# Optimization experiments

Measured on AMD Instinct MI355X. Metric: run time of the kernel, lower is better.

Reference implementation:

```python
import jax, jax.numpy as jnp
import numpy as np

N_NODES = 50000
N_EDGES = 800000
IN_DIM = 128
HID = 128
N_LAYERS = 3
N_CLASSES = 6
NUM_GRAPHS = 64
BN_EPS = 1e-5


def setup_inputs() -> dict:
    key = jax.random.key(0)
    ks = jax.random.split(key, 12)
    x = jax.random.normal(ks[0], (N_NODES, IN_DIM), dtype=jnp.float32)
    edge_index = jax.random.randint(ks[1], (2, N_EDGES), 0, N_NODES, dtype=jnp.int32)
    batch = jnp.sort(jax.random.randint(ks[2], (N_NODES,), 0, NUM_GRAPHS, dtype=jnp.int32))
    s = 1.0 / np.sqrt(HID)
    # stacked per-layer params (all layers are [HID, HID] since IN_DIM == HID)
    Wl = jax.random.uniform(ks[3], (N_LAYERS, HID, HID), jnp.float32, -s, s)  # lin_l (neighbor agg), has bias
    bl = jax.random.uniform(ks[4], (N_LAYERS, HID), jnp.float32, -s, s)
    Wr = jax.random.uniform(ks[5], (N_LAYERS, HID, HID), jnp.float32, -s, s)  # lin_r (root), no bias
    gamma = jnp.ones((N_LAYERS, HID), jnp.float32)
    beta = jnp.zeros((N_LAYERS, HID), jnp.float32)
    W1 = jax.random.uniform(ks[6], (HID // 2, HID), jnp.float32, -s, s)
    b1 = jax.random.uniform(ks[7], (HID // 2,), jnp.float32, -s, s)
    s2 = 1.0 / np.sqrt(HID // 2)
    W2 = jax.random.uniform(ks[8], (N_CLASSES, HID // 2), jnp.float32, -s2, s2)
    b2 = jax.random.uniform(ks[9], (N_CLASSES,), jnp.float32, -s2, s2)
    return {"x": x, "edge_index": edge_index, "batch": batch, "Wl": Wl, "bl": bl,
            "Wr": Wr, "gamma": gamma, "beta": beta, "W1": W1, "b1": b1, "W2": W2, "b2": b2}


def reference(x, edge_index, batch, Wl, bl, Wr, gamma, beta, W1, b1, W2, b2):
    src, dst = edge_index[0], edge_index[1]
    n = x.shape[0]
    # in-degree (for mean aggregation), computed once; clamp to avoid div-by-zero
    deg = jax.ops.segment_sum(jnp.ones((src.shape[0],), x.dtype), dst, num_segments=n)
    deg = jnp.maximum(deg, 1.0)[:, None]
    for l in range(N_LAYERS):
        # SAGEConv: mean-aggregate neighbor features, then lin_l(agg) + lin_r(x)
        agg = jax.ops.segment_sum(x[src], dst, num_segments=n) / deg  # [N, HID]
        h = agg @ Wl[l].T + bl[l] + x @ Wr[l].T
        # BatchNorm1d (training-mode batch statistics over nodes)
        mu = h.mean(axis=0)
        var = h.var(axis=0)
        h = (h - mu) * jax.lax.rsqrt(var + BN_EPS) * gamma[l] + beta[l]
        x = jax.nn.relu(h)  # dropout omitted (eval semantics / deterministic baseline)
    # global_mean_pool over graph ids
    pooled = jax.ops.segment_sum(x, batch, num_segments=NUM_GRAPHS)
    cnt = jax.ops.segment_sum(jnp.ones((n,), x.dtype), batch, num_segments=NUM_GRAPHS)
    pooled = pooled / jnp.maximum(cnt, 1.0)[:, None]
    # MLP head
    h = jax.nn.relu(pooled @ W1.T + b1)
    return h @ W2.T + b2
```

## Files before the change

### kernel.cpp

```cpp
#include <hip/hip_runtime.h>

#define N_NODES 50000
#define N_EDGES 800000
#define DIM 128
#define NLAYERS 3
#define NCLASSES 6
#define NGRAPHS 64
#define BN_EPS 1e-5f

#define SCAN_BLK 256
#define SCAN_NB ((N_NODES + SCAN_BLK - 1) / SCAN_BLK)

#define POOL_CHUNKS 8
#define NPART 16

#define FILL_GRPS 8
#define FILL_BPG 128
#define NODES_PER_GRP ((N_NODES + FILL_GRPS - 1) / FILL_GRPS)

typedef unsigned short ushort_t;
typedef unsigned int uint_t;
using bf16x8 = __attribute__((ext_vector_type(8))) short;
using f32x4 = __attribute__((ext_vector_type(4))) float;

__device__ __forceinline__ float bf2f(ushort_t b) {
  return __uint_as_float(((uint_t)b) << 16);
}
__device__ __forceinline__ ushort_t f2bf(float f) {
  uint_t u = __float_as_uint(f);
  u += 0x7fffu + ((u >> 16) & 1u);
  return (ushort_t)(u >> 16);
}


__global__ void k_count(const int* __restrict__ dst, int* __restrict__ cnt) {
  int e = blockIdx.x * blockDim.x + threadIdx.x;
  if (e < N_EDGES) atomicAdd(&cnt[dst[e]], 1);
}

__global__ void k_scan_a(const int* __restrict__ cnt, int* __restrict__ incl,
                         int* __restrict__ bsum) {
  __shared__ int s[SCAN_BLK];
  int i = blockIdx.x * SCAN_BLK + threadIdx.x;
  int v = (i < N_NODES) ? cnt[i] : 0;
  s[threadIdx.x] = v;
  __syncthreads();
  for (int off = 1; off < SCAN_BLK; off <<= 1) {
    int t = (threadIdx.x >= off) ? s[threadIdx.x - off] : 0;
    __syncthreads();
    s[threadIdx.x] += t;
    __syncthreads();
  }
  if (i < N_NODES) incl[i] = s[threadIdx.x];
  if (threadIdx.x == SCAN_BLK - 1) bsum[blockIdx.x] = s[SCAN_BLK - 1];
}

__global__ void k_scan_b(const int* __restrict__ bsum, int* __restrict__ boff) {
  __shared__ int s[SCAN_BLK];
  int t = threadIdx.x;
  int v = (t < SCAN_NB) ? bsum[t] : 0;
  s[t] = v;
  __syncthreads();
  for (int off = 1; off < SCAN_BLK; off <<= 1) {
    int u = (t >= off) ? s[t - off] : 0;
    __syncthreads();
    s[t] += u;
    __syncthreads();
  }
  boff[t] = s[t] - v;
}

__global__ void k_scan_c(const int* __restrict__ cnt, const int* __restrict__ incl,
                         const int* __restrict__ boff, int* __restrict__ row_ptr,
                         int* __restrict__ cursor, float* __restrict__ degf) {
  int i = blockIdx.x * SCAN_BLK + threadIdx.x;
  if (i < N_NODES) {
    int ex = incl[i] - cnt[i] + boff[blockIdx.x];
    row_ptr[i] = ex;
    cursor[i] = ex;
    degf[i] = (float)max(cnt[i], 1);
  }
  if (i == 0) row_ptr[N_NODES] = N_EDGES;
}

__global__ void k_fill2(const int* __restrict__ src, const int* __restrict__ dst,
                        int* __restrict__ cursor, int* __restrict__ col) {
  int grp = blockIdx.x & (FILL_GRPS - 1);
  int blk = blockIdx.x >> 3;
  int lo = grp * NODES_PER_GRP;
  int hi = min(lo + NODES_PER_GRP, N_NODES);
  int per = (N_EDGES + FILL_BPG - 1) / FILL_BPG;
  int es = blk * per, ee = min(es + per, N_EDGES);
  for (int e = es + (int)threadIdx.x; e < ee; e += (int)blockDim.x) {
    int d = dst[e];
    if (d >= lo && d < hi) {
      int pos = atomicAdd(&cursor[d], 1);
      col[pos] = src[e];
    }
  }
}

__global__ void k_wt2(const float* __restrict__ Wl, const float* __restrict__ Wr,
                      ushort_t* __restrict__ W2) {
  int i = blockIdx.x * blockDim.x + threadIdx.x;
  if (i >= NLAYERS * 8 * 4 * 128) return;
  int c = i & 127;
  int q = (i >> 7) & 3;
  int ks = (i >> 9) & 7;
  int l = i >> 12;
  int kbase = ks * 32 + q * 8;
  size_t obase = (size_t)l * 65536 + ks * 8192 + q * 1024 + c * 8;
#pragma unroll
  for (int kk = 0; kk < 8; ++kk) {
    int k = kbase + kk;
    float w = (k < DIM) ? Wl[(size_t)l * DIM * DIM + c * DIM + k]
                        : Wr[(size_t)l * DIM * DIM + c * DIM + (k - DIM)];
    ushort_t hi = f2bf(w);
    float lo = w - bf2f(hi);
    W2[obase + kk] = hi;
    W2[obase + 4096 + kk] = f2bf(lo);
  }
}

__global__ void k_tobf16(const float* __restrict__ x, ushort_t* __restrict__ xb) {
  int i4 = blockIdx.x * blockDim.x + threadIdx.x;
  if (i4 >= N_NODES * DIM / 4) return;
  float4 v = ((const float4*)x)[i4];
  ushort4 o;
  o.x = f2bf(v.x);
  o.y = f2bf(v.y);
  o.z = f2bf(v.z);
  o.w = f2bf(v.w);
  ((ushort4*)xb)[i4] = o;
}


__global__ void k_gather4(const ushort_t* __restrict__ xb, const int* __restrict__ row_ptr,
                          const int* __restrict__ col, const float* __restrict__ degf,
                          ushort_t* __restrict__ aggb) {
  int wid = threadIdx.x >> 6, lane = threadIdx.x & 63;
  int n = blockIdx.x * 4 + wid;
  if (n >= N_NODES) return;
  int beg = row_ptr[n], end = row_ptr[n + 1];
  int sub = lane >> 4;
  int c16 = lane & 15;
  const uint4* x4 = (const uint4*)xb;
  float a[8] = {0.f, 0.f, 0.f, 0.f, 0.f, 0.f, 0.f, 0.f};
  int p = beg + sub;
  for (; p + 12 < end; p += 16) {
    int c[4];
#pragma unroll
    for (int u = 0; u < 4; ++u) c[u] = col[p + 4 * u];
    uint4 v[4];
#pragma unroll
    for (int u = 0; u < 4; ++u) v[u] = x4[(size_t)c[u] * 16 + c16];
#pragma unroll
    for (int u = 0; u < 4; ++u) {
      a[0] += bf2f((ushort_t)(v[u].x & 0xffffu));
      a[1] += bf2f((ushort_t)(v[u].x >> 16));
      a[2] += bf2f((ushort_t)(v[u].y & 0xffffu));
      a[3] += bf2f((ushort_t)(v[u].y >> 16));
      a[4] += bf2f((ushort_t)(v[u].z & 0xffffu));
      a[5] += bf2f((ushort_t)(v[u].z >> 16));
      a[6] += bf2f((ushort_t)(v[u].w & 0xffffu));
      a[7] += bf2f((ushort_t)(v[u].w >> 16));
    }
  }
  for (; p < end; p += 4) {
    uint4 v = x4[(size_t)col[p] * 16 + c16];
    a[0] += bf2f((ushort_t)(v.x & 0xffffu));
    a[1] += bf2f((ushort_t)(v.x >> 16));
    a[2] += bf2f((ushort_t)(v.y & 0xffffu));
    a[3] += bf2f((ushort_t)(v.y >> 16));
    a[4] += bf2f((ushort_t)(v.z & 0xffffu));
    a[5] += bf2f((ushort_t)(v.z >> 16));
    a[6] += bf2f((ushort_t)(v.w & 0xffffu));
    a[7] += bf2f((ushort_t)(v.w >> 16));
  }
#pragma unroll
  for (int u = 0; u < 8; ++u) {
    a[u] += __shfl_xor(a[u], 16);
    a[u] += __shfl_xor(a[u], 32);
  }
  if (sub == 0) {
    float inv = 1.0f / degf[n];
    uint4 o;
    o.x = (uint_t)f2bf(a[0] * inv) | ((uint_t)f2bf(a[1] * inv) << 16);
    o.y = (uint_t)f2bf(a[2] * inv) | ((uint_t)f2bf(a[3] * inv) << 16);
    o.z = (uint_t)f2bf(a[4] * inv) | ((uint_t)f2bf(a[5] * inv) << 16);
    o.w = (uint_t)f2bf(a[6] * inv) | ((uint_t)f2bf(a[7] * inv) << 16);
    ((uint4*)aggb)[(size_t)n * 16 + c16] = o;
  }
}

__global__ __launch_bounds__(256) void k_mfma3(
    const ushort_t* __restrict__ aggb, const ushort_t* __restrict__ xb,
    const ushort_t* __restrict__ W2l, const float* __restrict__ bl,
    ushort_t* __restrict__ hb, float* __restrict__ sums_part) {
  __shared__ ushort_t Bs[16384];
  __shared__ float Es[4][16][65];
  __shared__ float lsums[4][256];

  int tid = threadIdx.x;
  int wave = tid >> 6, lane = tid & 63;
  int rw = blockIdx.x * 64 + wave * 16;
  int lr = lane & 15;
  int q = lane >> 4;
  int rowA = rw + lr;
  if (rowA > N_NODES - 1) rowA = N_NODES - 1;

  f32x4 acc[8];
#pragma unroll
  for (int c = 0; c < 8; ++c) acc[c] = (f32x4){0.f, 0.f, 0.f, 0.f};

#pragma unroll 1
  for (int kp = 0; kp < 4; ++kp) {
    const uint4* wsrc = (const uint4*)(W2l + (size_t)kp * 16384);
#pragma unroll
    for (int it = 0; it < 8; ++it)
      ((uint4*)Bs)[it * 256 + tid] = wsrc[it * 256 + tid];
    __syncthreads();
#pragma unroll
    for (int kh = 0; kh < 2; ++kh) {
      int ks = kp * 2 + kh;
      const ushort_t* Asrc = (ks < 4) ? aggb : xb;
      int koff = (ks & 3) * 32 + q * 8;
      bf16x8 af = *(const bf16x8*)(Asrc + (size_t)rowA * DIM + koff);
      const ushort_t* bbase = Bs + kh * 8192 + q * 1024;
#pragma unroll
      for (int cf = 0; cf < 8; ++cf) {
        int ci = cf * 16 + lr;
        bf16x8 bh = *(const bf16x8*)(bbase + ci * 8);
        bf16x8 bo = *(const bf16x8*)(bbase + 4096 + ci * 8);
        acc[cf] = __builtin_amdgcn_mfma_f32_16x16x32_bf16(af, bh, acc[cf], 0, 0, 0);
        acc[cf] = __builtin_amdgcn_mfma_f32_16x16x32_bf16(af, bo, acc[cf], 0, 0, 0);
      }
    }
    __syncthreads();
  }

  float ts[2][4] = {{0.f, 0.f, 0.f, 0.f}, {0.f, 0.f, 0.f, 0.f}};
  float tq[2][4] = {{0.f, 0.f, 0.f, 0.f}, {0.f, 0.f, 0.f, 0.f}};
#pragma unroll
  for (int colhalf = 0; colhalf < 2; ++colhalf) {
#pragma unroll
    for (int cf2 = 0; cf2 < 4; ++cf2) {
      f32x4 a = acc[colhalf * 4 + cf2];
#pragma unroll
      for (int i = 0; i < 4; ++i) Es[wave][q * 4 + i][cf2 * 16 + lr] = a[i];
    }
#pragma unroll
    for (int it = 0; it < 4; ++it) {
      int idx = it * 64 + lane;
      int r = idx >> 4, c4 = idx & 15;
      int n = rw + r;
      if (n < N_NODES) {
        int j = colhalf * 64 + c4 * 4;
        float4 v = *(float4*)&Es[wave][r][c4 * 4];
        v.x += bl[j];
        v.y += bl[j + 1];
        v.z += bl[j + 2];
        v.w += bl[j + 3];
        ts[colhalf][0] += v.x;
        ts[colhalf][1] += v.y;
        ts[colhalf][2] += v.z;
        ts[colhalf][3] += v.w;
        tq[colhalf][0] += v.x * v.x;
        tq[colhalf][1] += v.y * v.y;
        tq[colhalf][2] += v.z * v.z;
        tq[colhalf][3] += v.w * v.w;
        ushort4 o;
        o.x = f2bf(v.x);
        o.y = f2bf(v.y);
        o.z = f2bf(v.z);
        o.w = f2bf(v.w);
        *(ushort4*)(hb + (size_t)n * DIM + j) = o;
      }
    }
  }
#pragma unroll
  for (int ch = 0; ch < 2; ++ch)
#pragma unroll
    for (int u = 0; u < 4; ++u) {
      ts[ch][u] += __shfl_xor(ts[ch][u], 16);
      ts[ch][u] += __shfl_xor(ts[ch][u], 32);
      tq[ch][u] += __shfl_xor(tq[ch][u], 16);
      tq[ch][u] += __shfl_xor(tq[ch][u], 32);
    }
  if (lane < 16) {
#pragma unroll
    for (int ch = 0; ch < 2; ++ch)
#pragma unroll
      for (int u = 0; u < 4; ++u) {
        int j = ch * 64 + lr * 4 + u;
        lsums[wave][j] = ts[ch][u];
        lsums[wave][128 + j] = tq[ch][u];
      }
  }
  __syncthreads();
  float tot = lsums[0][tid] + lsums[1][tid] + lsums[2][tid] + lsums[3][tid];
  atomicAdd(&sums_part[(blockIdx.x & (NPART - 1)) * 256 + tid], tot);
}

__global__ void k_bnfin(const float* __restrict__ sums_part, const float* __restrict__ gamma,
                        const float* __restrict__ beta, float* __restrict__ bnsc) {
  int j = threadIdx.x;
  float s = 0.f, q = 0.f;
  for (int p = 0; p < NPART; ++p) {
    s += sums_part[p * 256 + j];
    q += sums_part[p * 256 + 128 + j];
  }
  float mu = s * (1.0f / N_NODES);
  float var = q * (1.0f / N_NODES) - mu * mu;
  float sc = gamma[j] * rsqrtf(var + BN_EPS);
  bnsc[j] = sc;
  bnsc[128 + j] = beta[j] - mu * sc;
}

__global__ void k_bn_apply2(const ushort_t* __restrict__ hb, const float* __restrict__ bnsc,
                            ushort_t* __restrict__ xb) {
  int i4 = blockIdx.x * blockDim.x + threadIdx.x;
  if (i4 >= N_NODES * DIM / 4) return;
  int j0 = (i4 * 4) & (DIM - 1);
  ushort4 v = ((const ushort4*)hb)[i4];
  float o[4] = {bf2f(v.x), bf2f(v.y), bf2f(v.z), bf2f(v.w)};
  ushort4 r;
#pragma unroll
  for (int u = 0; u < 4; ++u) {
    int j = j0 + u;
    o[u] = fmaxf(fmaf(o[u], bnsc[j], bnsc[128 + j]), 0.f);
  }
  r.x = f2bf(o[0]);
  r.y = f2bf(o[1]);
  r.z = f2bf(o[2]);
  r.w = f2bf(o[3]);
  ((ushort4*)xb)[i4] = r;
}


__global__ void k_gbounds(const int* __restrict__ batch, int* __restrict__ gstart) {
  int t = threadIdx.x;
  if (t > NGRAPHS) return;
  if (t == NGRAPHS) {
    gstart[NGRAPHS] = N_NODES;
    return;
  }
  int lo = 0, hi = N_NODES;
  while (lo < hi) {
    int mid = (lo + hi) >> 1;
    if (batch[mid] < t) lo = mid + 1;
    else hi = mid;
  }
  gstart[t] = lo;
}

__global__ void k_pool4(const ushort_t* __restrict__ hb, const float* __restrict__ bnsc,
                        const int* __restrict__ gstart, float* __restrict__ pooled) {
  int g = blockIdx.x >> 3;
  int ck = blockIdx.x & 7;
  int s = gstart[g], e = gstart[g + 1];
  int len = e - s;
  int per = (len + POOL_CHUNKS - 1) / POOL_CHUNKS;
  int rs = s + ck * per;
  int re = min(rs + per, e);
  int j2 = threadIdx.x & 63;
  int rg = threadIdx.x >> 6;
  const uint_t* h1 = (const uint_t*)hb;
  float sc0 = bnsc[2 * j2], sh0 = bnsc[128 + 2 * j2];
  float sc1 = bnsc[2 * j2 + 1], sh1 = bnsc[128 + 2 * j2 + 1];
  float ax = 0.f, ay = 0.f;
  for (int r = rs + rg; r < re; r += 4) {
    uint_t v = h1[(size_t)r * 64 + j2];
    ax += fmaxf(fmaf(bf2f((ushort_t)(v & 0xffffu)), sc0, sh0), 0.f);
    ay += fmaxf(fmaf(bf2f((ushort_t)(v >> 16)), sc1, sh1), 0.f);
  }
  __shared__ float sred[4][DIM];
  sred[rg][2 * j2] = ax;
  sred[rg][2 * j2 + 1] = ay;
  __syncthreads();
  if (rg < 2) {
    int j = rg * 64 + j2;
    float v = sred[0][j] + sred[1][j] + sred[2][j] + sred[3][j];
    atomicAdd(&pooled[g * DIM + j], v);
  }
}

__global__ void k_head2(const float* __restrict__ pooled, const int* __restrict__ gstart,
                        const float* __restrict__ W1, const float* __restrict__ b1,
                        const float* __restrict__ W2, const float* __restrict__ b2,
                        float* __restrict__ out) {
  int g = blockIdx.x;
  int tid = threadIdx.x;
  __shared__ float pm[DIM];
  __shared__ float hid[64];
  float inv = 1.0f / fmaxf((float)(gstart[g + 1] - gstart[g]), 1.0f);
  if (tid < DIM) pm[tid] = pooled[g * DIM + tid] * inv;
  __syncthreads();
  {
    int m = tid >> 2, part = tid & 3;
    const float* w = W1 + m * DIM + part * 32;
    const float* pp = pm + part * 32;
    float acc = 0.f;
#pragma unroll
    for (int k = 0; k < 32; ++k) acc += pp[k] * w[k];
    acc += __shfl_down(acc, 1);
    acc += __shfl_down(acc, 2);
    if (part == 0) hid[m] = fmaxf(acc + b1[m], 0.f);
  }
  __syncthreads();
  if (tid < NCLASSES * 8) {
    int c = tid >> 3, pp8 = tid & 7;
    const float* w = W2 + c * 64 + pp8 * 8;
    const float* hh = hid + pp8 * 8;
    float acc = 0.f;
#pragma unroll
    for (int k = 0; k < 8; ++k) acc += hh[k] * w[k];
    acc += __shfl_down(acc, 1);
    acc += __shfl_down(acc, 2);
    acc += __shfl_down(acc, 4);
    if (pp8 == 0) out[g * NCLASSES + c] = acc + b2[c];
  }
}


extern "C" void kernel_launch(void* const* d_in, const int* in_sizes, int n_in,
                              void* d_out, int out_size, void* d_ws, size_t ws_size,
                              hipStream_t stream) {
  const float* x = (const float*)d_in[0];
  const int* edge = (const int*)d_in[1];
  const int* batch = (const int*)d_in[2];
  const float* Wl = (const float*)d_in[3];
  const float* bl = (const float*)d_in[4];
  const float* Wr = (const float*)d_in[5];
  const float* gamma = (const float*)d_in[6];
  const float* beta = (const float*)d_in[7];
  const float* W1 = (const float*)d_in[8];
  const float* b1 = (const float*)d_in[9];
  const float* W2 = (const float*)d_in[10];
  const float* b2 = (const float*)d_in[11];
  float* out = (float*)d_out;

  const int* src = edge;
  const int* dst = edge + N_EDGES;

  char* p = (char*)d_ws;
  auto alloc = [&](size_t bytes) -> void* {
    void* r = (void*)p;
    p += (bytes + 255) & ~(size_t)255;
    return r;
  };
  int* cnt = (int*)alloc(N_NODES * 4);
  int* incl = (int*)alloc(N_NODES * 4);
  int* bsum = (int*)alloc(SCAN_BLK * 4);
  int* boff = (int*)alloc(SCAN_BLK * 4);
  int* row_ptr = (int*)alloc((N_NODES + 1) * 4);
  int* cursor = (int*)alloc(N_NODES * 4);
  int* col = (int*)alloc(N_EDGES * 4);
  float* degf = (float*)alloc(N_NODES * 4);
  ushort_t* W2b = (ushort_t*)alloc((size_t)NLAYERS * 65536 * 2);
  ushort_t* xb0 = (ushort_t*)alloc((size_t)N_NODES * DIM * 2);
  ushort_t* xb_cur = (ushort_t*)alloc((size_t)N_NODES * DIM * 2);
  ushort_t* aggb = (ushort_t*)alloc((size_t)N_NODES * DIM * 2);
  ushort_t* hb = (ushort_t*)alloc((size_t)N_NODES * DIM * 2);
  float* sums_part = (float*)alloc(NPART * 256 * 4);
  float* bnsc = (float*)alloc(2 * DIM * 4);
  float* pooled = (float*)alloc(NGRAPHS * DIM * 4);
  int* gstart = (int*)alloc((NGRAPHS + 1) * 4);

  hipMemsetAsync(cnt, 0, N_NODES * 4, stream);
  k_count<<<(N_EDGES + 255) / 256, 256, 0, stream>>>(dst, cnt);
  k_scan_a<<<SCAN_NB, SCAN_BLK, 0, stream>>>(cnt, incl, bsum);
  k_scan_b<<<1, SCAN_BLK, 0, stream>>>(bsum, boff);
  k_scan_c<<<SCAN_NB, SCAN_BLK, 0, stream>>>(cnt, incl, boff, row_ptr, cursor, degf);
  k_fill2<<<FILL_GRPS * FILL_BPG, 256, 0, stream>>>(src, dst, cursor, col);
  k_wt2<<<(NLAYERS * 8 * 4 * 128 + 255) / 256, 256, 0, stream>>>(Wl, Wr, W2b);
  k_gbounds<<<1, 128, 0, stream>>>(batch, gstart);
  k_tobf16<<<(N_NODES * DIM / 4 + 255) / 256, 256, 0, stream>>>(x, xb0);

  const ushort_t* xin = xb0;
  for (int l = 0; l < NLAYERS; ++l) {
    k_gather4<<<(N_NODES + 3) / 4, 256, 0, stream>>>(xin, row_ptr, col, degf, aggb);
    hipMemsetAsync(sums_part, 0, NPART * 256 * 4, stream);
    k_mfma3<<<(N_NODES + 63) / 64, 256, 0, stream>>>(
        aggb, xin, W2b + (size_t)l * 65536, bl + (size_t)l * DIM, hb, sums_part);
    k_bnfin<<<1, 128, 0, stream>>>(sums_part, gamma + (size_t)l * DIM,
                                   beta + (size_t)l * DIM, bnsc);
    if (l < NLAYERS - 1) {
      k_bn_apply2<<<(N_NODES * DIM / 4 + 255) / 256, 256, 0, stream>>>(hb, bnsc, xb_cur);
      xin = xb_cur;
    }
  }

  hipMemsetAsync(pooled, 0, NGRAPHS * DIM * 4, stream);
  k_pool4<<<NGRAPHS * POOL_CHUNKS, 256, 0, stream>>>(hb, bnsc, gstart, pooled);
  k_head2<<<NGRAPHS, 256, 0, stream>>>(pooled, gstart, W1, b1, W2, b2, out);
}
```

Before: 305.1 us.

## Fuse BN+ReLU into gather and root loads; XCD-aware ticketed CSR fill

```diff
diff --git a/kernel.cpp b/kernel.cpp
--- a/kernel.cpp
+++ b/kernel.cpp
@@ -15,7 +15,9 @@
 #define NPART 16
 
 #define FILL_GRPS 8
-#define FILL_BPG 128
+#define FILL_SLICES 128
+#define FILL_EPS ((N_EDGES + FILL_SLICES - 1) / FILL_SLICES)
+#define FILL_NB 2048
 #define NODES_PER_GRP ((N_NODES + FILL_GRPS - 1) / FILL_GRPS)
 
 typedef unsigned short ushort_t;
@@ -83,19 +85,29 @@
   if (i == 0) row_ptr[N_NODES] = N_EDGES;
 }
 
-__global__ void k_fill2(const int* __restrict__ src, const int* __restrict__ dst,
-                        int* __restrict__ cursor, int* __restrict__ col) {
-  int grp = blockIdx.x & (FILL_GRPS - 1);
-  int blk = blockIdx.x >> 3;
-  int lo = grp * NODES_PER_GRP;
+__global__ void k_fill3(const int* __restrict__ src, const int* __restrict__ dst,
+                        int* __restrict__ cursor, int* __restrict__ col,
+                        int* __restrict__ ticket) {
+  uint_t xcd;
+  asm("s_getreg_b32 %0, hwreg(HW_REG_XCC_ID)" : "=s"(xcd));
+  xcd &= 7;
+  int lo = (int)xcd * NODES_PER_GRP;
   int hi = min(lo + NODES_PER_GRP, N_NODES);
-  int per = (N_EDGES + FILL_BPG - 1) / FILL_BPG;
-  int es = blk * per, ee = min(es + per, N_EDGES);
-  for (int e = es + (int)threadIdx.x; e < ee; e += (int)blockDim.x) {
-    int d = dst[e];
-    if (d >= lo && d < hi) {
-      int pos = atomicAdd(&cursor[d], 1);
-      col[pos] = src[e];
+  __shared__ int s_slice;
+  for (;;) {
+    if (threadIdx.x == 0) s_slice = atomicAdd(&ticket[xcd], 1);
+    __syncthreads();
+    int slice = s_slice;
+    __syncthreads();
+    if (slice >= FILL_SLICES) break;
+    int es = slice * FILL_EPS;
+    int ee = min(es + FILL_EPS, N_EDGES);
+    for (int e = es + (int)threadIdx.x; e < ee; e += (int)blockDim.x) {
+      int d = dst[e];
+      if (d >= lo && d < hi) {
+        int pos = atomicAdd(&cursor[d], 1);
+        col[pos] = src[e];
+      }
     }
   }
 }
@@ -135,8 +147,25 @@
 }
 
 
+__device__ __forceinline__ void acc8(uint4 v, float* a, const float* sc,
+                                     const float* sh, bool ap) {
+  uint_t w[4] = {v.x, v.y, v.z, v.w};
+#pragma unroll
+  for (int u = 0; u < 4; ++u) {
+    float f0 = bf2f((ushort_t)(w[u] & 0xffffu));
+    float f1 = bf2f((ushort_t)(w[u] >> 16));
+    if (ap) {
+      f0 = fmaxf(fmaf(f0, sc[2 * u], sh[2 * u]), 0.f);
+      f1 = fmaxf(fmaf(f1, sc[2 * u + 1], sh[2 * u + 1]), 0.f);
+    }
+    a[2 * u] += f0;
+    a[2 * u + 1] += f1;
+  }
+}
+
 __global__ void k_gather4(const ushort_t* __restrict__ xb, const int* __restrict__ row_ptr,
                           const int* __restrict__ col, const float* __restrict__ degf,
+                          const float* __restrict__ bnsc, int apply,
                           ushort_t* __restrict__ aggb) {
   int wid = threadIdx.x >> 6, lane = threadIdx.x & 63;
   int n = blockIdx.x * 4 + wid;
@@ -145,6 +174,13 @@
   int sub = lane >> 4;
   int c16 = lane & 15;
   const uint4* x4 = (const uint4*)xb;
+  float sc[8], sh[8];
+#pragma unroll
+  for (int u = 0; u < 8; ++u) {
+    sc[u] = apply ? bnsc[8 * c16 + u] : 1.f;
+    sh[u] = apply ? bnsc[128 + 8 * c16 + u] : 0.f;
+  }
+  bool ap = apply != 0;
   float a[8] = {0.f, 0.f, 0.f, 0.f, 0.f, 0.f, 0.f, 0.f};
   int p = beg + sub;
   for (; p + 12 < end; p += 16) {
@@ -155,27 +191,11 @@
 #pragma unroll
     for (int u = 0; u < 4; ++u) v[u] = x4[(size_t)c[u] * 16 + c16];
 #pragma unroll
-    for (int u = 0; u < 4; ++u) {
-      a[0] += bf2f((ushort_t)(v[u].x & 0xffffu));
-      a[1] += bf2f((ushort_t)(v[u].x >> 16));
-      a[2] += bf2f((ushort_t)(v[u].y & 0xffffu));
-      a[3] += bf2f((ushort_t)(v[u].y >> 16));
-      a[4] += bf2f((ushort_t)(v[u].z & 0xffffu));
-      a[5] += bf2f((ushort_t)(v[u].z >> 16));
-      a[6] += bf2f((ushort_t)(v[u].w & 0xffffu));
-      a[7] += bf2f((ushort_t)(v[u].w >> 16));
-    }
+    for (int u = 0; u < 4; ++u) acc8(v[u], a, sc, sh, ap);
   }
   for (; p < end; p += 4) {
     uint4 v = x4[(size_t)col[p] * 16 + c16];
-    a[0] += bf2f((ushort_t)(v.x & 0xffffu));
-    a[1] += bf2f((ushort_t)(v.x >> 16));
-    a[2] += bf2f((ushort_t)(v.y & 0xffffu));
-    a[3] += bf2f((ushort_t)(v.y >> 16));
-    a[4] += bf2f((ushort_t)(v.z & 0xffffu));
-    a[5] += bf2f((ushort_t)(v.z >> 16));
-    a[6] += bf2f((ushort_t)(v.w & 0xffffu));
-    a[7] += bf2f((ushort_t)(v.w >> 16));
+    acc8(v, a, sc, sh, ap);
   }
 #pragma unroll
   for (int u = 0; u < 8; ++u) {
@@ -194,7 +214,8 @@
 }
 
 __global__ __launch_bounds__(256) void k_mfma3(
-    const ushort_t* __restrict__ aggb, const ushort_t* __restrict__ xb,
+    const ushort_t* __restrict__ aggb, const ushort_t* __restrict__ xroot,
+    const float* __restrict__ bnr, int rootApply,
     const ushort_t* __restrict__ W2l, const float* __restrict__ bl,
     ushort_t* __restrict__ hb, float* __restrict__ sums_part) {
   __shared__ ushort_t Bs[16384];
@@ -223,9 +244,21 @@
 #pragma unroll
     for (int kh = 0; kh < 2; ++kh) {
       int ks = kp * 2 + kh;
-      const ushort_t* Asrc = (ks < 4) ? aggb : xb;
       int koff = (ks & 3) * 32 + q * 8;
-      bf16x8 af = *(const bf16x8*)(Asrc + (size_t)rowA * DIM + koff);
+      bf16x8 af;
+      if (ks < 4) {
+        af = *(const bf16x8*)(aggb + (size_t)rowA * DIM + koff);
+      } else {
+        af = *(const bf16x8*)(xroot + (size_t)rowA * DIM + koff);
+        if (rootApply) {
+#pragma unroll
+          for (int u = 0; u < 8; ++u) {
+            float f = bf2f((ushort_t)af[u]);
+            f = fmaxf(fmaf(f, bnr[koff + u], bnr[128 + koff + u]), 0.f);
+            af[u] = (short)f2bf(f);
+          }
+        }
+      }
       const ushort_t* bbase = Bs + kh * 8192 + q * 1024;
 #pragma unroll
       for (int cf = 0; cf < 8; ++cf) {
@@ -302,39 +335,21 @@
   atomicAdd(&sums_part[(blockIdx.x & (NPART - 1)) * 256 + tid], tot);
 }
 
-__global__ void k_bnfin(const float* __restrict__ sums_part, const float* __restrict__ gamma,
+__global__ void k_bnfin(float* __restrict__ sums_part, const float* __restrict__ gamma,
                         const float* __restrict__ beta, float* __restrict__ bnsc) {
   int j = threadIdx.x;
   float s = 0.f, q = 0.f;
   for (int p = 0; p < NPART; ++p) {
     s += sums_part[p * 256 + j];
     q += sums_part[p * 256 + 128 + j];
+    sums_part[p * 256 + j] = 0.f;
+    sums_part[p * 256 + 128 + j] = 0.f;
   }
   float mu = s * (1.0f / N_NODES);
   float var = q * (1.0f / N_NODES) - mu * mu;
   float sc = gamma[j] * rsqrtf(var + BN_EPS);
   bnsc[j] = sc;
   bnsc[128 + j] = beta[j] - mu * sc;
-}
-
-__global__ void k_bn_apply2(const ushort_t* __restrict__ hb, const float* __restrict__ bnsc,
-                            ushort_t* __restrict__ xb) {
-  int i4 = blockIdx.x * blockDim.x + threadIdx.x;
-  if (i4 >= N_NODES * DIM / 4) return;
-  int j0 = (i4 * 4) & (DIM - 1);
-  ushort4 v = ((const ushort4*)hb)[i4];
-  float o[4] = {bf2f(v.x), bf2f(v.y), bf2f(v.z), bf2f(v.w)};
-  ushort4 r;
-#pragma unroll
-  for (int u = 0; u < 4; ++u) {
-    int j = j0 + u;
-    o[u] = fmaxf(fmaf(o[u], bnsc[j], bnsc[128 + j]), 0.f);
-  }
-  r.x = f2bf(o[0]);
-  r.y = f2bf(o[1]);
-  r.z = f2bf(o[2]);
-  r.w = f2bf(o[3]);
-  ((ushort4*)xb)[i4] = r;
 }
 
 
@@ -457,41 +472,46 @@
   int* cursor = (int*)alloc(N_NODES * 4);
   int* col = (int*)alloc(N_EDGES * 4);
   float* degf = (float*)alloc(N_NODES * 4);
+  int* ticket = (int*)alloc(FILL_GRPS * 4);
   ushort_t* W2b = (ushort_t*)alloc((size_t)NLAYERS * 65536 * 2);
   ushort_t* xb0 = (ushort_t*)alloc((size_t)N_NODES * DIM * 2);
-  ushort_t* xb_cur = (ushort_t*)alloc((size_t)N_NODES * DIM * 2);
+  ushort_t* hbA = (ushort_t*)alloc((size_t)N_NODES * DIM * 2);
+  ushort_t* hbB = (ushort_t*)alloc((size_t)N_NODES * DIM * 2);
   ushort_t* aggb = (ushort_t*)alloc((size_t)N_NODES * DIM * 2);
-  ushort_t* hb = (ushort_t*)alloc((size_t)N_NODES * DIM * 2);
   float* sums_part = (float*)alloc(NPART * 256 * 4);
   float* bnsc = (float*)alloc(2 * DIM * 4);
   float* pooled = (float*)alloc(NGRAPHS * DIM * 4);
   int* gstart = (int*)alloc((NGRAPHS + 1) * 4);
 
   hipMemsetAsync(cnt, 0, N_NODES * 4, stream);
+  hipMemsetAsync(ticket, 0, FILL_GRPS * 4, stream);
+  hipMemsetAsync(sums_part, 0, NPART * 256 * 4, stream);
   k_count<<<(N_EDGES + 255) / 256, 256, 0, stream>>>(dst, cnt);
   k_scan_a<<<SCAN_NB, SCAN_BLK, 0, stream>>>(cnt, incl, bsum);
   k_scan_b<<<1, SCAN_BLK, 0, stream>>>(bsum, boff);
   k_scan_c<<<SCAN_NB, SCAN_BLK, 0, stream>>>(cnt, incl, boff, row_ptr, cursor, degf);
-  k_fill2<<<FILL_GRPS * FILL_BPG, 256, 0, stream>>>(src, dst, cursor, col);
+  k_fill3<<<FILL_NB, 256, 0, stream>>>(src, dst, cursor, col, ticket);
   k_wt2<<<(NLAYERS * 8 * 4 * 128 + 255) / 256, 256, 0, stream>>>(Wl, Wr, W2b);
   k_gbounds<<<1, 128, 0, stream>>>(batch, gstart);
   k_tobf16<<<(N_NODES * DIM / 4 + 255) / 256, 256, 0, stream>>>(x, xb0);
 
   const ushort_t* xin = xb0;
+  ushort_t* hout = hbA;
   for (int l = 0; l < NLAYERS; ++l) {
-    k_gather4<<<(N_NODES + 3) / 4, 256, 0, stream>>>(xin, row_ptr, col, degf, aggb);
-    hipMemsetAsync(sums_part, 0, NPART * 256 * 4, stream);
+    int apply = (l > 0) ? 1 : 0;
+    k_gather4<<<(N_NODES + 3) / 4, 256, 0, stream>>>(xin, row_ptr, col, degf,
+                                                     bnsc, apply, aggb);
     k_mfma3<<<(N_NODES + 63) / 64, 256, 0, stream>>>(
-        aggb, xin, W2b + (size_t)l * 65536, bl + (size_t)l * DIM, hb, sums_part);
+        aggb, xin, bnsc, apply, W2b + (size_t)l * 65536, bl + (size_t)l * DIM,
+        hout, sums_part);
     k_bnfin<<<1, 128, 0, stream>>>(sums_part, gamma + (size_t)l * DIM,
                                    beta + (size_t)l * DIM, bnsc);
-    if (l < NLAYERS - 1) {
-      k_bn_apply2<<<(N_NODES * DIM / 4 + 255) / 256, 256, 0, stream>>>(hb, bnsc, xb_cur);
-      xin = xb_cur;
-    }
+    xin = hout;
+    hout = (hout == hbA) ? hbB : hbA;
   }
 
   hipMemsetAsync(pooled, 0, NGRAPHS * DIM * 4, stream);
-  k_pool4<<<NGRAPHS * POOL_CHUNKS, 256, 0, stream>>>(hb, bnsc, gstart, pooled);
+  k_pool4<<<NGRAPHS * POOL_CHUNKS, 256, 0, stream>>>((const ushort_t*)xin, bnsc,
+                                                     gstart, pooled);
   k_head2<<<NGRAPHS, 256, 0, stream>>>(pooled, gstart, W1, b1, W2, b2, out);
 }
```

Measured after the change: 483.0 us. +58.3%, slower.

## Bind CSR fill node ranges to XCD with dynamic slice tickets; fold BN partial reset

Applied to the files above, without the earlier changes.

```diff
diff --git a/kernel.cpp b/kernel.cpp
--- a/kernel.cpp
+++ b/kernel.cpp
@@ -15,7 +15,9 @@
 #define NPART 16
 
 #define FILL_GRPS 8
-#define FILL_BPG 128
+#define FILL_SLICES 128
+#define FILL_EPS ((N_EDGES + FILL_SLICES - 1) / FILL_SLICES)
+#define FILL_NB 2048
 #define NODES_PER_GRP ((N_NODES + FILL_GRPS - 1) / FILL_GRPS)
 
 typedef unsigned short ushort_t;
@@ -83,19 +85,29 @@
   if (i == 0) row_ptr[N_NODES] = N_EDGES;
 }
 
-__global__ void k_fill2(const int* __restrict__ src, const int* __restrict__ dst,
-                        int* __restrict__ cursor, int* __restrict__ col) {
-  int grp = blockIdx.x & (FILL_GRPS - 1);
-  int blk = blockIdx.x >> 3;
-  int lo = grp * NODES_PER_GRP;
+__global__ void k_fill3(const int* __restrict__ src, const int* __restrict__ dst,
+                        int* __restrict__ cursor, int* __restrict__ col,
+                        int* __restrict__ ticket) {
+  uint_t xcd;
+  asm("s_getreg_b32 %0, hwreg(HW_REG_XCC_ID)" : "=s"(xcd));
+  xcd &= 7;
+  int lo = (int)xcd * NODES_PER_GRP;
   int hi = min(lo + NODES_PER_GRP, N_NODES);
-  int per = (N_EDGES + FILL_BPG - 1) / FILL_BPG;
-  int es = blk * per, ee = min(es + per, N_EDGES);
-  for (int e = es + (int)threadIdx.x; e < ee; e += (int)blockDim.x) {
-    int d = dst[e];
-    if (d >= lo && d < hi) {
-      int pos = atomicAdd(&cursor[d], 1);
-      col[pos] = src[e];
+  __shared__ int s_slice;
+  for (;;) {
+    if (threadIdx.x == 0) s_slice = atomicAdd(&ticket[xcd], 1);
+    __syncthreads();
+    int slice = s_slice;
+    __syncthreads();
+    if (slice >= FILL_SLICES) break;
+    int es = slice * FILL_EPS;
+    int ee = min(es + FILL_EPS, N_EDGES);
+    for (int e = es + (int)threadIdx.x; e < ee; e += (int)blockDim.x) {
+      int d = dst[e];
+      if (d >= lo && d < hi) {
+        int pos = atomicAdd(&cursor[d], 1);
+        col[pos] = src[e];
+      }
     }
   }
 }
@@ -302,13 +314,15 @@
   atomicAdd(&sums_part[(blockIdx.x & (NPART - 1)) * 256 + tid], tot);
 }
 
-__global__ void k_bnfin(const float* __restrict__ sums_part, const float* __restrict__ gamma,
+__global__ void k_bnfin(float* __restrict__ sums_part, const float* __restrict__ gamma,
                         const float* __restrict__ beta, float* __restrict__ bnsc) {
   int j = threadIdx.x;
   float s = 0.f, q = 0.f;
   for (int p = 0; p < NPART; ++p) {
     s += sums_part[p * 256 + j];
     q += sums_part[p * 256 + 128 + j];
+    sums_part[p * 256 + j] = 0.f;
+    sums_part[p * 256 + 128 + j] = 0.f;
   }
   float mu = s * (1.0f / N_NODES);
   float var = q * (1.0f / N_NODES) - mu * mu;
@@ -457,6 +471,7 @@
   int* cursor = (int*)alloc(N_NODES * 4);
   int* col = (int*)alloc(N_EDGES * 4);
   float* degf = (float*)alloc(N_NODES * 4);
+  int* ticket = (int*)alloc(FILL_GRPS * 4);
   ushort_t* W2b = (ushort_t*)alloc((size_t)NLAYERS * 65536 * 2);
   ushort_t* xb0 = (ushort_t*)alloc((size_t)N_NODES * DIM * 2);
   ushort_t* xb_cur = (ushort_t*)alloc((size_t)N_NODES * DIM * 2);
@@ -468,11 +483,13 @@
   int* gstart = (int*)alloc((NGRAPHS + 1) * 4);
 
   hipMemsetAsync(cnt, 0, N_NODES * 4, stream);
+  hipMemsetAsync(ticket, 0, FILL_GRPS * 4, stream);
+  hipMemsetAsync(sums_part, 0, NPART * 256 * 4, stream);
   k_count<<<(N_EDGES + 255) / 256, 256, 0, stream>>>(dst, cnt);
   k_scan_a<<<SCAN_NB, SCAN_BLK, 0, stream>>>(cnt, incl, bsum);
   k_scan_b<<<1, SCAN_BLK, 0, stream>>>(bsum, boff);
   k_scan_c<<<SCAN_NB, SCAN_BLK, 0, stream>>>(cnt, incl, boff, row_ptr, cursor, degf);
-  k_fill2<<<FILL_GRPS * FILL_BPG, 256, 0, stream>>>(src, dst, cursor, col);
+  k_fill3<<<FILL_NB, 256, 0, stream>>>(src, dst, cursor, col, ticket);
   k_wt2<<<(NLAYERS * 8 * 4 * 128 + 255) / 256, 256, 0, stream>>>(Wl, Wr, W2b);
   k_gbounds<<<1, 128, 0, stream>>>(batch, gstart);
   k_tobf16<<<(N_NODES * DIM / 4 + 255) / 256, 256, 0, stream>>>(x, xb0);
@@ -480,7 +497,6 @@
   const ushort_t* xin = xb0;
   for (int l = 0; l < NLAYERS; ++l) {
     k_gather4<<<(N_NODES + 3) / 4, 256, 0, stream>>>(xin, row_ptr, col, degf, aggb);
-    hipMemsetAsync(sums_part, 0, NPART * 256 * 4, stream);
     k_mfma3<<<(N_NODES + 63) / 64, 256, 0, stream>>>(
         aggb, xin, W2b + (size_t)l * 65536, bl + (size_t)l * DIM, hb, sums_part);
     k_bnfin<<<1, 128, 0, stream>>>(sums_part, gamma + (size_t)l * DIM,
```

Measured after the change: 331.5 us. 1.09x slower.
